# Kernel optimization log

Measured on AMD Instinct MI355X. Metric: run time of the kernel, lower is better.

## Reference

```python
import jax, jax.numpy as jnp
import numpy as np

N = 16384
IN_DIM = 64
OUT_DIM = 64
BN_EPS = 1e-5
LEAKY_SLOPE = 0.01


def setup_inputs() -> dict:
    key = jax.random.key(0)
    k_g, k_h, k_w, k_b = jax.random.split(key, 4)
    g = jax.random.uniform(k_g, (N, N), dtype=jnp.float32)  # dense nonneg adjacency
    h = jax.random.normal(k_h, (N, IN_DIM), dtype=jnp.float32)
    W = jax.random.normal(k_w, (OUT_DIM, IN_DIM), dtype=jnp.float32) * (1.0 / np.sqrt(IN_DIM))
    b = jax.random.normal(k_b, (OUT_DIM,), dtype=jnp.float32) * 0.01
    gamma = jnp.ones((IN_DIM,), dtype=jnp.float32)
    beta = jnp.zeros((IN_DIM,), dtype=jnp.float32)
    return {"g": g, "h": h, "W": W, "b": b, "gamma": gamma, "beta": beta}


def reference(g, h, W, b, gamma, beta):
    # BatchNorm1d in training mode: batch statistics over the node axis
    mean = h.mean(axis=0)
    var = jnp.mean(jnp.square(h - mean), axis=0)  # biased variance, as torch BN
    hn = (h - mean) * (gamma / jnp.sqrt(var + BN_EPS)) + beta

    # g <- g + I  (add self-loops on the diagonal, no dense eye materialized)
    idx = jnp.arange(g.shape[0])
    ga = g.at[idx, idx].add(1.0)

    # D^{-1/2} A D^{-1/2}: torch builds diag matrices and does two N^3 matmuls;
    # mathematically identical row/column scaling (same values, O(N^2)).
    d_inv_sqrt = jax.lax.rsqrt(ga.sum(axis=1))  # [N]
    gn = ga * d_inv_sqrt[:, None] * d_inv_sqrt[None, :]

    # Linear projection, propagate, LeakyReLU
    hp = hn @ W.T + b                     # [N, out_dim]
    out = gn @ hp                         # [N, out_dim]
    return jnp.where(out >= 0, out, LEAKY_SLOPE * out)
```

## Files before the change

kernel.cpp:

```cpp
#include <hip/hip_runtime.h>
#include <hip/hip_bf16.h>

#define GN 16384
#define GDIM 64

typedef __attribute__((ext_vector_type(8))) short bf16x8;
typedef __attribute__((ext_vector_type(4))) float f32x4;

typedef __attribute__((address_space(1))) const void GASV;
typedef __attribute__((address_space(3))) void LASV;

template <typename T>
__device__ __forceinline__ T ntl(const T* p) { return __builtin_nontemporal_load(p); }
template <typename T>
__device__ __forceinline__ void nts(T v, T* p) { __builtin_nontemporal_store(v, p); }

__device__ __forceinline__ unsigned short f2bf(float x) {
    unsigned int u = __builtin_bit_cast(unsigned int, x);
    u += 0x7fffu + ((u >> 16) & 1u);
    return (unsigned short)(u >> 16);
}

__device__ __forceinline__ short f2bf_hw(float x) {
    __hip_bfloat16 b = __float2bfloat16(x);
    return (short)__builtin_bit_cast(unsigned short, b);
}

__global__ void bn_partial(const float* __restrict__ h, float* __restrict__ ps,
                           float* __restrict__ pq) {
    int b = blockIdx.x, t = threadIdx.x;
    int col = t & 63, wr = t >> 6;
    float s = 0.f, q = 0.f;
    int base = b * 64;
    for (int rep = 0; rep < 16; ++rep) {
        int row = base + wr + rep * 4;
        float v = h[row * GDIM + col];
        s += v; q += v * v;
    }
    __shared__ float ls[4][64], lq[4][64];
    ls[wr][col] = s; lq[wr][col] = q;
    __syncthreads();
    if (t < 64) {
        ps[b * 64 + t] = ls[0][t] + ls[1][t] + ls[2][t] + ls[3][t];
        pq[b * 64 + t] = lq[0][t] + lq[1][t] + lq[2][t] + lq[3][t];
    }
}

__global__ void bn_finalize(const float* __restrict__ ps, const float* __restrict__ pq,
                            const float* __restrict__ W, const float* __restrict__ bvec,
                            const float* __restrict__ gamma, const float* __restrict__ beta,
                            float* __restrict__ Wp, float* __restrict__ bp) {
    int t = threadIdx.x;
    __shared__ float s_s[64], s_t2[64];
    if (t < 64) {
        float S = 0.f, Q = 0.f;
        for (int b = 0; b < 256; ++b) { S += ps[b * 64 + t]; Q += pq[b * 64 + t]; }
        float mean = S * (1.0f / 16384.0f);
        float var  = Q * (1.0f / 16384.0f) - mean * mean;
        float sc   = gamma[t] * rsqrtf(var + 1e-5f);
        s_s[t]  = sc;
        s_t2[t] = beta[t] - mean * sc;
    }
    __syncthreads();
    for (int k = 0; k < 16; ++k) {
        int idx = t + k * 256;
        Wp[idx] = s_s[idx & 63] * W[idx];
    }
    if (t < 64) {
        float acc = bvec[t];
        for (int c = 0; c < 64; ++c) acc += s_t2[c] * W[t * 64 + c];
        bp[t] = acc;
    }
}

__global__ void linear_hp(const float* __restrict__ h, const float* __restrict__ Wp,
                          const float* __restrict__ bpr, float* __restrict__ hp) {
    __shared__ float lw[64][65];
    __shared__ float lh[16][65];
    int t = threadIdx.x;
    int rb = blockIdx.x * 16;
    for (int k = 0; k < 16; ++k) {
        int idx = t + k * 256;
        lw[idx >> 6][idx & 63] = Wp[idx];
    }
    for (int k = 0; k < 4; ++k) {
        int idx = t + k * 256;
        lh[idx >> 6][idx & 63] = h[rb * GDIM + idx];
    }
    __syncthreads();
    int o = t & 63, rg = t >> 6;
    float a0 = 0.f, a1 = 0.f, a2 = 0.f, a3 = 0.f;
    for (int c = 0; c < 64; ++c) {
        float wv = lw[o][c];
        a0 += lh[rg][c]      * wv;
        a1 += lh[rg + 4][c]  * wv;
        a2 += lh[rg + 8][c]  * wv;
        a3 += lh[rg + 12][c] * wv;
    }
    float bb = bpr[o];
    hp[(rb + rg) * GDIM + o]      = a0 + bb;
    hp[(rb + rg + 4) * GDIM + o]  = a1 + bb;
    hp[(rb + rg + 8) * GDIM + o]  = a2 + bb;
    hp[(rb + rg + 12) * GDIM + o] = a3 + bb;
}

__global__ void rowsum_dinv(const float* __restrict__ g, float* __restrict__ dinv) {
    int row = blockIdx.x, t = threadIdx.x;
    const f32x4* grow = (const f32x4*)(g + (size_t)row * GN);
    float s = 0.f;
    for (int k = 0; k < 16; ++k) {
        f32x4 v = ntl(grow + t + k * 256);
        s += (v[0] + v[1]) + (v[2] + v[3]);
    }
    for (int off = 32; off; off >>= 1) s += __shfl_down(s, off, 64);
    __shared__ float wsum[4];
    if ((t & 63) == 0) wsum[t >> 6] = s;
    __syncthreads();
    if (t == 0) {
        float tot = (wsum[0] + wsum[1]) + (wsum[2] + wsum[3]) + 1.0f;
        dinv[row] = rsqrtf(tot);
    }
}

__global__ void make_hsT(const float* __restrict__ hp, const float* __restrict__ dinv,
                         unsigned short* __restrict__ hsT) {
    __shared__ float tile[64][65];
    int t = threadIdx.x;
    int jb = blockIdx.x * 64;
    int o = t & 63, jg = t >> 6;
    for (int k = 0; k < 16; ++k) {
        int j = jg + k * 4;
        tile[j][o] = hp[(jb + j) * GDIM + o] * dinv[jb + j];
    }
    __syncthreads();
    int oo = t >> 2, q = t & 3;
    for (int k = 0; k < 16; ++k) {
        int j = q * 16 + k;
        hsT[(size_t)oo * GN + jb + j] = f2bf(tile[j][oo]);
    }
}

__global__ void __launch_bounds__(512, 2) spmm_part(
    const float* __restrict__ g, const unsigned short* __restrict__ hsT,
    float* __restrict__ part)
{
    __shared__ unsigned short bs[2][64][520];

    int t = threadIdx.x;
    int lane = t & 63;
    int w = t >> 6;
    int itile = blockIdx.x >> 2;
    int split = blockIdx.x & 3;
    int rb = itile * 256;
    int kb = split * 4096;
    int l15 = lane & 15;
    int kg = lane >> 4;

    f32x4 acc[2][4];
    #pragma unroll
    for (int m = 0; m < 2; ++m)
        #pragma unroll
        for (int n = 0; n < 4; ++n)
            #pragma unroll
            for (int r = 0; r < 4; ++r) acc[m][n][r] = 0.f;

    const float* abase = g + (size_t)(rb + w * 32 + l15) * GN + kb + kg * 8;

    auto stage = [&](int kc, int buf) {
        int ck = kb + kc * 512;
        #pragma unroll
        for (int q = 0; q < 8; ++q) {
            int o = w * 8 + q;
            const char* src = (const char*)(hsT + (size_t)o * GN + ck) + lane * 16;
            __builtin_amdgcn_global_load_lds((GASV*)src, (LASV*)&bs[buf][o][0], 16, 0, 0);
        }
    };

    stage(0, 0);
    __syncthreads();

    for (int c = 0; c < 8; ++c) {
        int buf = c & 1;
        if (c < 7) stage(c + 1, buf ^ 1);

        int cbase = c * 512;
        for (int it = 0; it < 16; ++it) {
            int ko = it * 32 + kg * 8;
            bf16x8 bfr[4];
            #pragma unroll
            for (int n = 0; n < 4; ++n)
                bfr[n] = *(const bf16x8*)&bs[buf][n * 16 + l15][ko];
            #pragma unroll
            for (int m = 0; m < 2; ++m) {
                const float* ap = abase + (size_t)m * 16 * GN + cbase + it * 32;
                f32x4 x0 = ntl((const f32x4*)ap);
                f32x4 x1 = ntl((const f32x4*)ap + 1);
                bf16x8 afr;
                afr[0] = f2bf_hw(x0[0]); afr[1] = f2bf_hw(x0[1]);
                afr[2] = f2bf_hw(x0[2]); afr[3] = f2bf_hw(x0[3]);
                afr[4] = f2bf_hw(x1[0]); afr[5] = f2bf_hw(x1[1]);
                afr[6] = f2bf_hw(x1[2]); afr[7] = f2bf_hw(x1[3]);
                #pragma unroll
                for (int n = 0; n < 4; ++n)
                    acc[m][n] = __builtin_amdgcn_mfma_f32_16x16x32_bf16(afr, bfr[n], acc[m][n], 0, 0, 0);
            }
        }
        __syncthreads();
    }

    float* pdst = part + (size_t)split * (GN * GDIM);
    #pragma unroll
    for (int m = 0; m < 2; ++m)
        #pragma unroll
        for (int n = 0; n < 4; ++n)
            #pragma unroll
            for (int r = 0; r < 4; ++r) {
                int i = rb + w * 32 + m * 16 + kg * 4 + r;
                int col = n * 16 + l15;
                nts(acc[m][n][r], &pdst[(size_t)i * GDIM + col]);
            }
}

__global__ void epilogue(const float* __restrict__ part, const float* __restrict__ hp,
                         const float* __restrict__ dinv, float* __restrict__ out) {
    int q = blockIdx.x * 256 + threadIdx.x;
    int i = q >> 4;
    int o = (q & 15) * 4;
    size_t off = (size_t)i * GDIM + o;
    const size_t S = (size_t)GN * GDIM;
    f32x4 s0 = ntl((const f32x4*)(part + off));
    f32x4 s1 = ntl((const f32x4*)(part + S + off));
    f32x4 s2 = ntl((const f32x4*)(part + 2 * S + off));
    f32x4 s3 = ntl((const f32x4*)(part + 3 * S + off));
    f32x4 hpv = *(const f32x4*)(hp + off);
    float di = dinv[i];
    f32x4 v = (s0 + s1) + (s2 + s3);
    #pragma unroll
    for (int r = 0; r < 4; ++r) {
        float x = di * (v[r] + di * hpv[r]);
        v[r] = (x >= 0.f) ? x : 0.01f * x;
    }
    nts(v, (f32x4*)(out + off));
}

extern "C" void kernel_launch(void* const* d_in, const int* in_sizes, int n_in,
                              void* d_out, int out_size, void* d_ws, size_t ws_size,
                              hipStream_t stream) {
    const float* g     = (const float*)d_in[0];
    const float* h     = (const float*)d_in[1];
    const float* W     = (const float*)d_in[2];
    const float* b     = (const float*)d_in[3];
    const float* gamma = (const float*)d_in[4];
    const float* beta  = (const float*)d_in[5];
    float* out = (float*)d_out;

    float* ws   = (float*)d_ws;
    float* ps   = ws;
    float* pq   = ws + 16384;
    float* Wp   = ws + 32768;
    float* bp   = ws + 36864;
    float* dinv = ws + 36928;
    float* hp   = ws + 53312;
    unsigned short* hsT = (unsigned short*)(ws + 1101888);
    float* part = ws + 1626176;

    bn_partial  <<<256,   256, 0, stream>>>(h, ps, pq);
    bn_finalize <<<1,     256, 0, stream>>>(ps, pq, W, b, gamma, beta, Wp, bp);
    linear_hp   <<<1024,  256, 0, stream>>>(h, Wp, bp, hp);
    rowsum_dinv <<<16384, 256, 0, stream>>>(g, dinv);
    make_hsT    <<<256,   256, 0, stream>>>(hp, dinv, hsT);
    spmm_part   <<<256,   512, 0, stream>>>(g, hsT, part);
    epilogue    <<<1024,  256, 0, stream>>>(part, hp, dinv, out);
}
```

Measured before the change: 454.4 us.

## Use 1024-thread spmm blocks, stagger k-chunks, drop nontemporal hints

```diff
diff --git a/kernel.cpp b/kernel.cpp
--- a/kernel.cpp
+++ b/kernel.cpp
@@ -9,11 +9,6 @@
 
 typedef __attribute__((address_space(1))) const void GASV;
 typedef __attribute__((address_space(3))) void LASV;
-
-template <typename T>
-__device__ __forceinline__ T ntl(const T* p) { return __builtin_nontemporal_load(p); }
-template <typename T>
-__device__ __forceinline__ void nts(T v, T* p) { __builtin_nontemporal_store(v, p); }
 
 __device__ __forceinline__ unsigned short f2bf(float x) {
     unsigned int u = __builtin_bit_cast(unsigned int, x);
@@ -109,7 +104,7 @@
     const f32x4* grow = (const f32x4*)(g + (size_t)row * GN);
     float s = 0.f;
     for (int k = 0; k < 16; ++k) {
-        f32x4 v = ntl(grow + t + k * 256);
+        f32x4 v = grow[t + k * 256];
         s += (v[0] + v[1]) + (v[2] + v[3]);
     }
     for (int off = 32; off; off >>= 1) s += __shfl_down(s, off, 64);
@@ -140,7 +135,7 @@
     }
 }
 
-__global__ void __launch_bounds__(512, 2) spmm_part(
+__global__ void __launch_bounds__(1024, 4) spmm_part(
     const float* __restrict__ g, const unsigned short* __restrict__ hsT,
     float* __restrict__ part)
 {
@@ -156,69 +151,63 @@
     int l15 = lane & 15;
     int kg = lane >> 4;
 
-    f32x4 acc[2][4];
+    f32x4 acc[4];
     #pragma unroll
-    for (int m = 0; m < 2; ++m)
+    for (int n = 0; n < 4; ++n)
         #pragma unroll
-        for (int n = 0; n < 4; ++n)
-            #pragma unroll
-            for (int r = 0; r < 4; ++r) acc[m][n][r] = 0.f;
-
-    const float* abase = g + (size_t)(rb + w * 32 + l15) * GN + kb + kg * 8;
+        for (int r = 0; r < 4; ++r) acc[n][r] = 0.f;
+
+    const float* abase = g + (size_t)(rb + w * 16 + l15) * GN + kb + kg * 8;
 
     auto stage = [&](int kc, int buf) {
         int ck = kb + kc * 512;
         #pragma unroll
-        for (int q = 0; q < 8; ++q) {
-            int o = w * 8 + q;
+        for (int q = 0; q < 4; ++q) {
+            int o = w * 4 + q;
             const char* src = (const char*)(hsT + (size_t)o * GN + ck) + lane * 16;
             __builtin_amdgcn_global_load_lds((GASV*)src, (LASV*)&bs[buf][o][0], 16, 0, 0);
         }
     };
 
-    stage(0, 0);
+    int c0 = itile & 7;
+    stage(c0, 0);
     __syncthreads();
 
     for (int c = 0; c < 8; ++c) {
         int buf = c & 1;
-        if (c < 7) stage(c + 1, buf ^ 1);
-
-        int cbase = c * 512;
+        if (c < 7) stage((c + 1 + itile) & 7, buf ^ 1);
+
+        int cbase = ((c + itile) & 7) * 512;
         for (int it = 0; it < 16; ++it) {
             int ko = it * 32 + kg * 8;
             bf16x8 bfr[4];
             #pragma unroll
             for (int n = 0; n < 4; ++n)
                 bfr[n] = *(const bf16x8*)&bs[buf][n * 16 + l15][ko];
+            const float* ap = abase + cbase + it * 32;
+            f32x4 x0 = *(const f32x4*)ap;
+            f32x4 x1 = *((const f32x4*)ap + 1);
+            bf16x8 afr;
+            afr[0] = f2bf_hw(x0[0]); afr[1] = f2bf_hw(x0[1]);
+            afr[2] = f2bf_hw(x0[2]); afr[3] = f2bf_hw(x0[3]);
+            afr[4] = f2bf_hw(x1[0]); afr[5] = f2bf_hw(x1[1]);
+            afr[6] = f2bf_hw(x1[2]); afr[7] = f2bf_hw(x1[3]);
             #pragma unroll
-            for (int m = 0; m < 2; ++m) {
-                const float* ap = abase + (size_t)m * 16 * GN + cbase + it * 32;
-                f32x4 x0 = ntl((const f32x4*)ap);
-                f32x4 x1 = ntl((const f32x4*)ap + 1);
-                bf16x8 afr;
-                afr[0] = f2bf_hw(x0[0]); afr[1] = f2bf_hw(x0[1]);
-                afr[2] = f2bf_hw(x0[2]); afr[3] = f2bf_hw(x0[3]);
-                afr[4] = f2bf_hw(x1[0]); afr[5] = f2bf_hw(x1[1]);
-                afr[6] = f2bf_hw(x1[2]); afr[7] = f2bf_hw(x1[3]);
-                #pragma unroll
-                for (int n = 0; n < 4; ++n)
-                    acc[m][n] = __builtin_amdgcn_mfma_f32_16x16x32_bf16(afr, bfr[n], acc[m][n], 0, 0, 0);
-            }
+            for (int n = 0; n < 4; ++n)
+                acc[n] = __builtin_amdgcn_mfma_f32_16x16x32_bf16(afr, bfr[n], acc[n], 0, 0, 0);
         }
         __syncthreads();
     }
 
     float* pdst = part + (size_t)split * (GN * GDIM);
     #pragma unroll
-    for (int m = 0; m < 2; ++m)
+    for (int n = 0; n < 4; ++n)
         #pragma unroll
-        for (int n = 0; n < 4; ++n)
-            #pragma unroll
-            for (int r = 0; r < 4; ++r) {
-                int i = rb + w * 32 + m * 16 + kg * 4 + r;
-                int col = n * 16 + l15;
-                nts(acc[m][n][r], &pdst[(size_t)i * GDIM + col]);
-            }
+        for (int r = 0; r < 4; ++r) {
+            int i = rb + w * 16 + kg * 4 + r;
+            int col = n * 16 + l15;
+            pdst[(size_t)i * GDIM + col] = acc[n][r];
+        }
 }
 
 __global__ void epilogue(const float* __restrict__ part, const float* __restrict__ hp,
@@ -228,10 +217,10 @@
     int o = (q & 15) * 4;
     size_t off = (size_t)i * GDIM + o;
     const size_t S = (size_t)GN * GDIM;
-    f32x4 s0 = ntl((const f32x4*)(part + off));
-    f32x4 s1 = ntl((const f32x4*)(part + S + off));
-    f32x4 s2 = ntl((const f32x4*)(part + 2 * S + off));
-    f32x4 s3 = ntl((const f32x4*)(part + 3 * S + off));
+    f32x4 s0 = *(const f32x4*)(part + off);
+    f32x4 s1 = *(const f32x4*)(part + S + off);
+    f32x4 s2 = *(const f32x4*)(part + 2 * S + off);
+    f32x4 s3 = *(const f32x4*)(part + 3 * S + off);
     f32x4 hpv = *(const f32x4*)(hp + off);
     float di = dinv[i];
     f32x4 v = (s0 + s1) + (s2 + s3);
@@ -240,7 +229,7 @@
         float x = di * (v[r] + di * hpv[r]);
         v[r] = (x >= 0.f) ? x : 0.01f * x;
     }
-    nts(v, (f32x4*)(out + off));
+    *(f32x4*)(out + off) = v;
 }
 
 extern "C" void kernel_launch(void* const* d_in, const int* in_sizes, int n_in,
@@ -269,6 +258,6 @@
     linear_hp   <<<1024,  256, 0, stream>>>(h, Wp, bp, hp);
     rowsum_dinv <<<16384, 256, 0, stream>>>(g, dinv);
     make_hsT    <<<256,   256, 0, stream>>>(hp, dinv, hsT);
-    spmm_part   <<<256,   512, 0, stream>>>(g, hsT, part);
+    spmm_part   <<<256,  1024, 0, stream>>>(g, hsT, part);
     epilogue    <<<1024,  256, 0, stream>>>(part, hp, dinv, out);
 }
```

Result: faster. 400.2 us (-11.9%).
